# Kernel tuning notes

Measured on AMD Instinct MI355X. Metric: run time of the kernel, lower is better.

The kernel has to match this reference:

```python
import jax, jax.numpy as jnp
import numpy as np

N, T = 8192, 256
SIGMA = 100.0
ALPHA = 1.0


def setup_inputs() -> dict:
    key = jax.random.key(0)
    k1, k2, k3 = jax.random.split(key, 3)
    # per-time-bin event probabilities: rows sum to 0.9 so cumsum (CDF) stays < 1
    p = jax.random.uniform(k1, (N, T), dtype=jnp.float32) + 1e-3
    y_pred = 0.9 * p / jnp.sum(p, axis=1, keepdims=True)
    y = jax.random.randint(k2, (N,), 0, T, dtype=jnp.int64)
    status = jax.random.randint(k3, (N,), 0, 2).astype(jnp.float32)
    return {"y_pred": y_pred, "y": y, "status": status}


def reference(y_pred, y, status):
    # F1[i, t] = CDF of predicted event time
    F1 = jnp.cumsum(y_pred, axis=1)                                   # [N, T]
    y_col = y[:, None]
    p_at_y = jnp.take_along_axis(y_pred, y_col, axis=1)[:, 0]         # y_pred[i, y[i]]
    A = jnp.take_along_axis(F1, y_col, axis=1)[:, 0]                  # F1[i, y[i]]
    # negative log-likelihood term
    L1 = -jnp.dot(jnp.log(p_at_y), status) - jnp.dot(jnp.log(1.0 - A), 1.0 - status)
    # pairwise ranking term: for i,j with status==1 and y[i] < y[j],
    # diff = F1[i, y[i]] - F1[j, y[i]]
    B = F1[:, y].T                                                    # B[i, j] = F1[j, y[i]]
    ev = status > 0.5
    M = (y[:, None] < y[None, :]) & ev[:, None] & ev[None, :]         # [N, N]
    L2 = ALPHA * jnp.sum(jnp.where(M, jnp.exp(-(A[:, None] - B) / SIGMA), 0.0))
    return L1 + L2
```

## Files before the change

kernel.cpp:

```cpp
#include <hip/hip_runtime.h>

#define NROWS 8192
#define TCOLS 256
#define NBLK  512
#define NREP  32
constexpr float SIGMA_INV = 0.01f;

__global__ __launch_bounds__(256) void surv_fused(
    const float* __restrict__ yp, const int* __restrict__ y,
    const float* __restrict__ st,
    float* __restrict__ G,
    float* __restrict__ H,
    float* __restrict__ l1acc,
    unsigned int* __restrict__ cnt,
    float* __restrict__ out)
{
    __shared__ float Gw[4][4][64];
    __shared__ float wl1[4];
    __shared__ float wsum[4];
    __shared__ unsigned int isLast;

    const int tid  = threadIdx.x;
    const int wave = tid >> 6;
    const int lane = tid & 63;
    const int rep  = blockIdx.x & (NREP - 1);

    Gw[wave][0][lane] = 0.f;
    Gw[wave][1][lane] = 0.f;
    Gw[wave][2][lane] = 0.f;
    Gw[wave][3][lane] = 0.f;

    const int row0 = blockIdx.x * 16 + wave * 4;

    float4 v[4];
    int    yv[4];
    float  sv[4];
    #pragma unroll
    for (int r = 0; r < 4; ++r) {
        v[r]  = reinterpret_cast<const float4*>(yp + (size_t)(row0 + r) * TCOLS)[lane];
        yv[r] = y[row0 + r];
        sv[r] = st[row0 + r];
    }

    float l1 = 0.f;
    #pragma unroll
    for (int r = 0; r < 4; ++r) {
        const float s0 = v[r].x;
        const float s1 = s0 + v[r].y;
        const float s2 = s1 + v[r].z;
        const float s3 = s2 + v[r].w;

        float x = s3;
        #pragma unroll
        for (int d = 1; d < 64; d <<= 1) {
            const float t = __shfl_up(x, d);
            if (lane >= d) x += t;
        }
        const float pre = x - s3;
        const float f0 = pre + s0, f1 = pre + s1, f2 = pre + s2, f3 = pre + s3;

        const int   yi  = yv[r];
        const float sti = sv[r];
        const bool  ev  = (sti > 0.5f);

        const int yl = yi >> 2, ye = yi & 3;
        const float fa = (ye == 0) ? f0 : (ye == 1) ? f1 : (ye == 2) ? f2 : f3;
        const float va = (ye == 0) ? v[r].x : (ye == 1) ? v[r].y
                       : (ye == 2) ? v[r].z : v[r].w;
        const float A = __shfl(fa, yl);
        const float p = __shfl(va, yl);

        if (lane == 0) {
            l1 += -sti * __logf(p) - (1.f - sti) * __logf(1.f - A);
            if (ev) atomicAdd(&H[rep * TCOLS + yi], __expf(-A * SIGMA_INV));
        }

        if (ev) {
            const int k0 = lane << 2;
            if (k0     < yi) Gw[wave][0][lane] += __expf(f0 * SIGMA_INV);
            if (k0 + 1 < yi) Gw[wave][1][lane] += __expf(f1 * SIGMA_INV);
            if (k0 + 2 < yi) Gw[wave][2][lane] += __expf(f2 * SIGMA_INV);
            if (k0 + 3 < yi) Gw[wave][3][lane] += __expf(f3 * SIGMA_INV);
        }
    }

    if (lane == 0) wl1[wave] = l1;
    __syncthreads();

    const float g = Gw[0][tid & 3][tid >> 2] + Gw[1][tid & 3][tid >> 2]
                  + Gw[2][tid & 3][tid >> 2] + Gw[3][tid & 3][tid >> 2];
    atomicAdd(&G[rep * TCOLS + tid], g);
    if (tid == 0) atomicAdd(&l1acc[rep * 16], wl1[0] + wl1[1] + wl1[2] + wl1[3]);

    __syncthreads();
    if (tid == 0) {
        const unsigned int old = atomicAdd(cnt, 1u);
        isLast = (old == 0xAAAAAAAAu + (NBLK - 1u)) || (old == NBLK - 1u);
    }
    __syncthreads();
    if (!isLast) return;

    float ga = 0.f, ha = 0.f;
    #pragma unroll
    for (int c = 0; c < NREP; ++c) {
        ga += __hip_atomic_load(&G[c * TCOLS + tid], __ATOMIC_RELAXED, __HIP_MEMORY_SCOPE_AGENT);
        ha += __hip_atomic_load(&H[c * TCOLS + tid], __ATOMIC_RELAXED, __HIP_MEMORY_SCOPE_AGENT);
    }
    float s = ga * ha;

    #pragma unroll
    for (int d = 32; d; d >>= 1) s += __shfl_down(s, d);
    if ((tid & 63) == 0) wsum[tid >> 6] = s;
    __syncthreads();
    if (tid == 0) {
        float l1s = 0.f;
        #pragma unroll
        for (int c = 0; c < NREP; ++c)
            l1s += __hip_atomic_load(&l1acc[c * 16], __ATOMIC_RELAXED, __HIP_MEMORY_SCOPE_AGENT);
        out[0] = wsum[0] + wsum[1] + wsum[2] + wsum[3] + l1s;
    }
}

extern "C" void kernel_launch(void* const* d_in, const int* in_sizes, int n_in,
                              void* d_out, int out_size, void* d_ws, size_t ws_size,
                              hipStream_t stream) {
    const float* yp = (const float*)d_in[0];
    const int*   y  = (const int*)d_in[1];
    const float* st = (const float*)d_in[2];

    char* ws = (char*)d_ws;
    float*        G     = (float*)ws;
    float*        H     = (float*)(ws + 32768);
    float*        l1acc = (float*)(ws + 65536);
    unsigned int* cnt   = (unsigned int*)(ws + 67584);
    float*        out   = (float*)d_out;

    surv_fused<<<NBLK, 256, 0, stream>>>(yp, y, st, G, H, l1acc, cnt, out);
}
```

Baseline: 68.82 us.

## Use 1024-thread blocks and register accumulators to cut global atomic traffic

Blocks grow from 256 to 1024 threads (16 waves, 64 rows each), so there are 128 blocks instead of 512. Each block's partial G vector is now reduced in shared memory before being added to global memory, which means four times fewer global atomics on G and l1acc. Per-wave G partials are kept in registers rather than read-modify-written in LDS for every row. The cost is fewer blocks than the GPU has compute units, which may lower memory-level parallelism, plus a longer serial LDS reduction over 16 waves.

```diff
diff --git a/kernel.cpp b/kernel.cpp
--- a/kernel.cpp
+++ b/kernel.cpp
@@ -2,11 +2,12 @@
 
 #define NROWS 8192
 #define TCOLS 256
-#define NBLK  512
+#define NBLK  128
+#define WAVES 16
 #define NREP  32
 constexpr float SIGMA_INV = 0.01f;
 
-__global__ __launch_bounds__(256) void surv_fused(
+__global__ __launch_bounds__(1024) void surv_fused(
     const float* __restrict__ yp, const int* __restrict__ y,
     const float* __restrict__ st,
     float* __restrict__ G,
@@ -15,8 +16,8 @@
     unsigned int* __restrict__ cnt,
     float* __restrict__ out)
 {
-    __shared__ float Gw[4][4][64];
-    __shared__ float wl1[4];
+    __shared__ float Gw[WAVES][4][64];
+    __shared__ float wl1[WAVES];
     __shared__ float wsum[4];
     __shared__ unsigned int isLast;
 
@@ -25,12 +26,7 @@
     const int lane = tid & 63;
     const int rep  = blockIdx.x & (NREP - 1);
 
-    Gw[wave][0][lane] = 0.f;
-    Gw[wave][1][lane] = 0.f;
-    Gw[wave][2][lane] = 0.f;
-    Gw[wave][3][lane] = 0.f;
-
-    const int row0 = blockIdx.x * 16 + wave * 4;
+    const int row0 = blockIdx.x * 64 + wave * 4;
 
     float4 v[4];
     int    yv[4];
@@ -42,6 +38,7 @@
         sv[r] = st[row0 + r];
     }
 
+    float g0 = 0.f, g1 = 0.f, g2 = 0.f, g3 = 0.f;
     float l1 = 0.f;
     #pragma unroll
     for (int r = 0; r < 4; ++r) {
@@ -77,20 +74,33 @@
 
         if (ev) {
             const int k0 = lane << 2;
-            if (k0     < yi) Gw[wave][0][lane] += __expf(f0 * SIGMA_INV);
-            if (k0 + 1 < yi) Gw[wave][1][lane] += __expf(f1 * SIGMA_INV);
-            if (k0 + 2 < yi) Gw[wave][2][lane] += __expf(f2 * SIGMA_INV);
-            if (k0 + 3 < yi) Gw[wave][3][lane] += __expf(f3 * SIGMA_INV);
+            if (k0     < yi) g0 += __expf(f0 * SIGMA_INV);
+            if (k0 + 1 < yi) g1 += __expf(f1 * SIGMA_INV);
+            if (k0 + 2 < yi) g2 += __expf(f2 * SIGMA_INV);
+            if (k0 + 3 < yi) g3 += __expf(f3 * SIGMA_INV);
         }
     }
 
+    Gw[wave][0][lane] = g0;
+    Gw[wave][1][lane] = g1;
+    Gw[wave][2][lane] = g2;
+    Gw[wave][3][lane] = g3;
     if (lane == 0) wl1[wave] = l1;
     __syncthreads();
 
-    const float g = Gw[0][tid & 3][tid >> 2] + Gw[1][tid & 3][tid >> 2]
-                  + Gw[2][tid & 3][tid >> 2] + Gw[3][tid & 3][tid >> 2];
-    atomicAdd(&G[rep * TCOLS + tid], g);
-    if (tid == 0) atomicAdd(&l1acc[rep * 16], wl1[0] + wl1[1] + wl1[2] + wl1[3]);
+    if (tid < TCOLS) {
+        float gsum = 0.f;
+        #pragma unroll
+        for (int w = 0; w < WAVES; ++w)
+            gsum += Gw[w][tid & 3][tid >> 2];
+        atomicAdd(&G[rep * TCOLS + tid], gsum);
+        if (tid == 0) {
+            float l1s = 0.f;
+            #pragma unroll
+            for (int w = 0; w < WAVES; ++w) l1s += wl1[w];
+            atomicAdd(&l1acc[rep * 16], l1s);
+        }
+    }
 
     __syncthreads();
     if (tid == 0) {
@@ -100,17 +110,18 @@
     __syncthreads();
     if (!isLast) return;
 
-    float ga = 0.f, ha = 0.f;
-    #pragma unroll
-    for (int c = 0; c < NREP; ++c) {
-        ga += __hip_atomic_load(&G[c * TCOLS + tid], __ATOMIC_RELAXED, __HIP_MEMORY_SCOPE_AGENT);
-        ha += __hip_atomic_load(&H[c * TCOLS + tid], __ATOMIC_RELAXED, __HIP_MEMORY_SCOPE_AGENT);
+    if (tid < TCOLS) {
+        float ga = 0.f, ha = 0.f;
+        #pragma unroll
+        for (int c = 0; c < NREP; ++c) {
+            ga += __hip_atomic_load(&G[c * TCOLS + tid], __ATOMIC_RELAXED, __HIP_MEMORY_SCOPE_AGENT);
+            ha += __hip_atomic_load(&H[c * TCOLS + tid], __ATOMIC_RELAXED, __HIP_MEMORY_SCOPE_AGENT);
+        }
+        float s = ga * ha;
+        #pragma unroll
+        for (int d = 32; d; d >>= 1) s += __shfl_down(s, d);
+        if ((tid & 63) == 0) wsum[tid >> 6] = s;
     }
-    float s = ga * ha;
-
-    #pragma unroll
-    for (int d = 32; d; d >>= 1) s += __shfl_down(s, d);
-    if ((tid & 63) == 0) wsum[tid >> 6] = s;
     __syncthreads();
     if (tid == 0) {
         float l1s = 0.f;
@@ -135,5 +146,5 @@
     unsigned int* cnt   = (unsigned int*)(ws + 67584);
     float*        out   = (float*)d_out;
 
-    surv_fused<<<NBLK, 256, 0, stream>>>(yp, y, st, G, H, l1acc, cnt, out);
+    surv_fused<<<NBLK, 1024, 0, stream>>>(yp, y, st, G, H, l1acc, cnt, out);
 }
```

After: 65.29 us. 5.1% less time.
